# Kernel tuning notes

Measured on AMD Instinct MI355X. Metric: run time of the kernel, lower is better.

## Reference

```python
import jax, jax.numpy as jnp
import numpy as np

KS = 3  # kernel size (mask semantics hardcode 3x3 = 9 taps)


def _xy2d(n, x, y):
    # Hilbert curve: 2D coords -> 1D distance (exact port of HilbertTopology.xy2d)
    d = 0
    s = n // 2
    while s > 0:
        rx = 1 if (x & s) > 0 else 0
        ry = 1 if (y & s) > 0 else 0
        d += s * s * ((3 * rx) ^ ry)
        # rot(s, x, y, rx, ry)
        if ry == 0:
            if rx == 1:
                x = s - 1 - x
                y = s - 1 - y
            x, y = y, x
        s //= 2
    return d


def _build_causal_mask(height, width):
    n = 1
    while n < max(width, height):
        n *= 2
    hgrid = np.empty((height, width), dtype=np.int64)
    for y in range(height):
        for x in range(width):
            hgrid[y, x] = _xy2d(n, x, y)
    # pad with -1 so out-of-bounds neighbors never mask (mask stays 1.0, matching torch code)
    hp = np.pad(hgrid, 1, constant_values=-1)
    mask = np.ones((KS * KS, height, width), dtype=np.float32)
    k = 0
    for dy in range(KS):
        for dx in range(KS):
            nh = hp[dy:dy + height, dx:dx + width]
            mask[k] = np.where(nh > hgrid, 0.0, 1.0)
            k += 1
    return mask[None, None]  # [1, 1, 9, H, W]


def setup_inputs() -> dict:
    key = jax.random.key(0)
    k1, k2 = jax.random.split(key)
    B, C, H, W = 4, 256, 128, 128
    retina = jax.random.normal(k1, (B, C, H, W), dtype=jnp.float32)
    evolve_weight = jax.random.normal(k2, (C, C, KS, KS), dtype=jnp.float32) * 0.05
    causal_mask = jnp.asarray(_build_causal_mask(H, W))
    return {"retina": retina, "evolve_weight": evolve_weight,
            "causal_mask": causal_mask, "steps": 5}


def _spatial_causal_conv(x, evolve_weight, causal_mask):
    B, C, H, W = x.shape
    xp = jnp.pad(x, ((0, 0), (0, 0), (1, 1), (1, 1)))
    # im2col in F.unfold's (dy, dx) tap order -> [B, C, 9, H, W]
    patches = jnp.stack([xp[:, :, dy:dy + H, dx:dx + W]
                         for dy in range(KS) for dx in range(KS)], axis=2)
    masked = patches * causal_mask  # position-dependent causal mask
    w = evolve_weight.reshape(C, C * KS * KS)
    out = jnp.einsum('oj,bjhw->bohw', w, masked.reshape(B, C * KS * KS, H, W))
    return out


def reference(retina, evolve_weight, causal_mask, steps):
    x = retina
    for _ in range(steps):
        delta = _spatial_causal_conv(x, evolve_weight, causal_mask)
        x = x + delta / (1.0 + jnp.abs(delta))  # exact_activation
    return x
```

## Files before the change

kernel.cpp:

```cpp
#include <hip/hip_runtime.h>
#include <math.h>
#include <stdint.h>

#define B_ 4
#define C_ 256
#define H_ 128
#define W_ 128
#define NPIX (H_*W_)

typedef short bf16x8 __attribute__((ext_vector_type(8)));
typedef int   i32x4  __attribute__((ext_vector_type(4)));
typedef float f32x4  __attribute__((ext_vector_type(4)));
typedef float f32x16 __attribute__((ext_vector_type(16)));
typedef unsigned short u16x4 __attribute__((ext_vector_type(4)));

#define XSZ   45056
#define WOFF  XSZ
#define WSL   16384
#define LDS_TOTAL (WOFF + 2*WSL)

__device__ __forceinline__ unsigned short f2bf_rne(float v) {
    uint32_t b = __float_as_uint(v);
    return (unsigned short)((b + 0x7fff + ((b >> 16) & 1)) >> 16);
}
__device__ __forceinline__ float bf2f(unsigned short h) {
    return __uint_as_float(((uint32_t)h) << 16);
}

__global__ __launch_bounds__(256)
void prep_w4(const float* __restrict__ wg, unsigned short* __restrict__ wb4,
             unsigned short* __restrict__ zb) {
    if (blockIdx.x == 2304) { if (threadIdx.x < 128) zb[threadIdx.x] = 0; return; }
    int f = blockIdx.x * 256 + threadIdx.x;
    int s2 = f >> 13;
    int r = f & 8191;
    int o_loc = r >> 6;
    int t = r & 63;
    int up = t >> 3, e = t & 7;
    int oh = s2 / 36, sl = s2 - oh * 36;
    int qt = sl / 9, k = sl - qt * 9;
    int u = up ^ (o_loc & 7);
    int c = qt * 64 + u * 8 + e;
    int o = oh * 128 + o_loc;
    wb4[f] = f2bf_rne(wg[(o * C_ + c) * 9 + k]);
}

__global__ __launch_bounds__(256)
void prep_split(const float* __restrict__ retina, unsigned short* __restrict__ hi,
                unsigned short* __restrict__ lo) {
    __shared__ unsigned int t[64][65];
    int bid = blockIdx.x;
    const int wt = bid & 1;        bid >>= 1;
    const int h  = bid & 127;      bid >>= 7;
    const int ct = bid & 3;        const int b = bid >> 2;
    const int tid = threadIdx.x;
    const int ci4 = tid >> 6, wi = tid & 63;
    #pragma unroll
    for (int cc = 0; cc < 16; ++cc) {
        int c_loc = cc * 4 + ci4;
        float v = retina[((size_t)(b * C_ + ct * 64 + c_loc) * H_ + h) * W_ + wt * 64 + wi];
        unsigned short hv = f2bf_rne(v);
        unsigned short lv = f2bf_rne(v - bf2f(hv));
        t[c_loc][wi] = (unsigned)hv | ((unsigned)lv << 16);
    }
    __syncthreads();
    const int p = tid >> 2, j = tid & 3;
    size_t base = (((size_t)(b * H_ + h) * W_ + wt * 64 + p) << 8) + ct * 64 + j * 16;
    u16x4 hv4[4], lv4[4];
    #pragma unroll
    for (int e = 0; e < 16; ++e) {
        unsigned u = t[j * 16 + e][p];
        hv4[e >> 2][e & 3] = (unsigned short)(u & 0xffffu);
        lv4[e >> 2][e & 3] = (unsigned short)(u >> 16);
    }
    #pragma unroll
    for (int q2 = 0; q2 < 4; ++q2) {
        *(u16x4*)(hi + base + q2 * 4) = hv4[q2];
        *(u16x4*)(lo + base + q2 * 4) = lv4[q2];
    }
}

__device__ __forceinline__ void stage_w(const unsigned short* __restrict__ wb4,
                                        char* smem, int woff, int oh, int sl,
                                        int wid, int l) {
    const char* src = (const char*)wb4 + ((size_t)(oh * 36 + sl) << 14);
    #pragma unroll
    for (int j = 0; j < 4; ++j) {
        const int seg = ((j << 2) + wid) << 10;
        __builtin_amdgcn_global_load_lds(
            (const __attribute__((address_space(1))) uint32_t*)(src + seg + l * 16),
            (__attribute__((address_space(3))) uint32_t*)(smem + woff + seg), 16, 0, 0);
    }
    __builtin_amdgcn_sched_barrier(0);
}

__device__ __forceinline__ void stage_x(const unsigned short* __restrict__ hi_in,
                                        const unsigned short* __restrict__ zb,
                                        char* smem, int b, int tr, int tc,
                                        int qt, int wid, int l) {
    const int slot_r = l >> 3, sub = l & 7;
    #pragma unroll
    for (int op = 0; op < 11; ++op) {
        const int sbase = (op << 5) + (wid << 3);
        const int s = sbase + slot_r;
        const int rr = (s * 3641) >> 16;
        const int hc = s - rr * 18;
        const int h = tr * 16 + rr - 1;
        const int w = tc * 16 + hc - 1;
        const unsigned short* src;
        if (s < 324 && (unsigned)h < 128u && (unsigned)w < 128u)
            src = hi_in + (((size_t)((b * 128 + h) * 128 + w)) << 8) + (qt << 6)
                        + ((sub ^ (s & 7)) << 3);
        else
            src = zb + (sub << 3);
        __builtin_amdgcn_global_load_lds(
            (const __attribute__((address_space(1))) uint32_t*)src,
            (__attribute__((address_space(3))) uint32_t*)(smem + (sbase << 7)),
            16, 0, 0);
    }
    __builtin_amdgcn_sched_barrier(0);
}

__global__ __launch_bounds__(256, 2)
void nca_v10(const unsigned short* __restrict__ hi_in,
             const unsigned short* __restrict__ lo_in,
             const unsigned short* __restrict__ wb4,
             const unsigned short* __restrict__ zb,
             const float* __restrict__ mask,
             unsigned short* __restrict__ hi_out,
             unsigned short* __restrict__ lo_out)
{
    extern __shared__ char smem[];
    const int tid = threadIdx.x;
    const int l = tid & 63, wid = tid >> 6;
    const int wave_o = wid & 1, wp = wid >> 1;
    const int lane31 = l & 31, khalf = l >> 5;
    const int col = l & 15, rowin = (l >> 4) & 1;

    int bid = blockIdx.x;
    const int oh = bid & 1; bid >>= 1;
    const int tc = bid & 7; bid >>= 3;
    const int tr = bid & 7; const int b = bid >> 3;

    unsigned long long mbits = 0ull;
    #pragma unroll
    for (int k = 0; k < 9; ++k) {
        #pragma unroll
        for (int n = 0; n < 4; ++n) {
            const int h = tr * 16 + wp * 8 + n * 2 + rowin;
            const int w = tc * 16 + col;
            unsigned long long bit = (mask[k * NPIX + h * W_ + w] != 0.f) ? 1ull : 0ull;
            mbits |= bit << (k * 4 + n);
        }
    }
    __builtin_amdgcn_sched_barrier(0);

    stage_x(hi_in, zb, smem, b, tr, tc, 0, wid, l);
    stage_w(wb4, smem, WOFF,       oh, 0, wid, l);
    stage_w(wb4, smem, WOFF + WSL, oh, 1, wid, l);

    int sB[4];
    #pragma unroll
    for (int n = 0; n < 4; ++n) sB[n] = (wp * 8 + n * 2 + rowin) * 18 + col;
    int abase[2], aswz[2];
    #pragma unroll
    for (int mo = 0; mo < 2; ++mo) {
        int o_l = wave_o * 64 + mo * 32 + lane31;
        abase[mo] = o_l << 7;
        aswz[mo] = o_l & 7;
    }

    f32x16 zv;
    #pragma unroll
    for (int r = 0; r < 16; ++r) zv[r] = 0.f;
    f32x16 acc[2][4];
    #pragma unroll
    for (int mo = 0; mo < 2; ++mo)
        #pragma unroll
        for (int n = 0; n < 4; ++n) acc[mo][n] = zv;

    #pragma unroll 1
    for (int qt = 0; qt < 4; ++qt) {
        #pragma unroll 1
        for (int k = 0; k < 9; ++k) {
            const int sl = qt * 9 + k;
            if (sl == 35) asm volatile("s_waitcnt vmcnt(0)" ::: "memory");
            else          asm volatile("s_waitcnt vmcnt(4)" ::: "memory");
            __builtin_amdgcn_sched_barrier(0);
            __builtin_amdgcn_s_barrier();

            const int dy = (k * 11) >> 5;
            const int dx = k - dy * 3;
            const int doff = dy * 18 + dx;
            const char* wbuf = smem + WOFF + ((sl & 1) ? WSL : 0);
            const unsigned mk = (unsigned)(mbits >> (k * 4));

            int sx[4];
            #pragma unroll
            for (int n = 0; n < 4; ++n) sx[n] = sB[n] + doff;

            __builtin_amdgcn_s_setprio(1);
            #pragma unroll
            for (int ks = 0; ks < 4; ++ks) {
                const int u = ks * 2 + khalf;
                bf16x8 av[2];
                #pragma unroll
                for (int mo = 0; mo < 2; ++mo)
                    av[mo] = *(const bf16x8*)(wbuf + abase[mo] + ((u ^ aswz[mo]) << 4));
                bf16x8 bv[4];
                #pragma unroll
                for (int n = 0; n < 4; ++n) {
                    i32x4 braw = *(const i32x4*)(smem + (sx[n] << 7) + ((u ^ (sx[n] & 7)) << 4));
                    const int mm = -(int)((mk >> n) & 1u);
                    #pragma unroll
                    for (int w4 = 0; w4 < 4; ++w4) braw[w4] &= mm;
                    bv[n] = __builtin_bit_cast(bf16x8, braw);
                }
                #pragma unroll
                for (int mo = 0; mo < 2; ++mo)
                    #pragma unroll
                    for (int n = 0; n < 4; ++n)
                        acc[mo][n] = __builtin_amdgcn_mfma_f32_32x32x16_bf16(av[mo], bv[n], acc[mo][n], 0, 0, 0);
            }
            __builtin_amdgcn_s_setprio(0);

            asm volatile("" ::: "memory");
            __builtin_amdgcn_s_barrier();
            if (k == 8 && qt < 3)
                stage_x(hi_in, zb, smem, b, tr, tc, qt + 1, wid, l);
            if (sl + 2 < 36)
                stage_w(wb4, smem, WOFF + ((sl & 1) ? WSL : 0), oh, sl + 2, wid, l);
        }
    }

    __syncthreads();
    #pragma unroll 1
    for (int ph = 0; ph < 2; ++ph) {
        #pragma unroll
        for (int n1 = 0; n1 < 2; ++n1) {
            const int n = ph * 2 + n1;
            const int pxp = (wp * 4 + n1 * 2 + ((l & 31) >> 4)) * 16 + col;
            #pragma unroll
            for (int mo = 0; mo < 2; ++mo)
                #pragma unroll
                for (int rq = 0; rq < 4; ++rq) {
                    const int u = wave_o * 16 + mo * 8 + rq * 2 + khalf;
                    f32x4 v;
                    v[0] = acc[mo][n][rq * 4 + 0];
                    v[1] = acc[mo][n][rq * 4 + 1];
                    v[2] = acc[mo][n][rq * 4 + 2];
                    v[3] = acc[mo][n][rq * 4 + 3];
                    *(f32x4*)(smem + pxp * 512 + ((u >> 3) << 7)
                              + ((((u & 7) ^ (u >> 3) ^ (pxp & 7))) << 4)) = v;
                }
        }
        __syncthreads();
        #pragma unroll 2
        for (int it = 0; it < 16; ++it) {
            const int pxp = it * 8 + wid * 2 + (l >> 5);
            const int u = l & 31;
            const f32x4 d4 = *(const f32x4*)(smem + pxp * 512 + ((u >> 3) << 7)
                                             + ((((u & 7) ^ (u >> 3) ^ (pxp & 7))) << 4));
            const int rp = pxp >> 4;
            const int h = tr * 16 + (rp >> 2) * 8 + ph * 4 + (rp & 3);
            const int w = tc * 16 + (pxp & 15);
            const size_t a2 = (((size_t)((b * 128 + h) * 128 + w)) << 8)
                              + (oh << 7) + (size_t)u * 4;
            const u16x4 h4 = *(const u16x4*)(hi_in + a2);
            const u16x4 l4 = *(const u16x4*)(lo_in + a2);
            u16x4 ho, lo2;
            #pragma unroll
            for (int r = 0; r < 4; ++r) {
                const float xv = bf2f(h4[r]) + bf2f(l4[r]);
                const float d = d4[r];
                const float xn = xv + d / (1.f + fabsf(d));
                ho[r] = f2bf_rne(xn);
                lo2[r] = f2bf_rne(xn - bf2f(ho[r]));
            }
            *(u16x4*)(hi_out + a2) = ho;
            *(u16x4*)(lo_out + a2) = lo2;
        }
        if (ph == 0) __syncthreads();
    }
}

__global__ __launch_bounds__(256)
void shadows_to_f32(const unsigned short* __restrict__ hi,
                    const unsigned short* __restrict__ lo,
                    float* __restrict__ out)
{
    __shared__ float t[64][132];
    int bid = blockIdx.x;
    const int ct = bid & 3;  bid >>= 2;
    const int h  = bid & 127; const int b = bid >> 7;
    const int tid = threadIdx.x;
    #pragma unroll
    for (int pass = 0; pass < 8; ++pass) {
        const int w = pass * 16 + (tid >> 4);
        const int c0 = (tid & 15) * 4;
        const size_t base = (((size_t)((b * 128 + h) * 128 + w)) << 8) + ct * 64 + c0;
        const u16x4 hv = *(const u16x4*)(hi + base);
        const u16x4 lv = *(const u16x4*)(lo + base);
        #pragma unroll
        for (int e = 0; e < 4; ++e) t[c0 + e][w] = bf2f(hv[e]) + bf2f(lv[e]);
    }
    __syncthreads();
    #pragma unroll
    for (int pass = 0; pass < 8; ++pass) {
        const int c = pass * 8 + (tid >> 5);
        const int w = (tid & 31) * 4;
        float4 v = make_float4(t[c][w], t[c][w + 1], t[c][w + 2], t[c][w + 3]);
        *(float4*)(out + ((size_t)(b * C_ + ct * 64 + c) * H_ + h) * W_ + w) = v;
    }
}

#define OT 64
#define TR 4
#define TC 16
#define CKC 16
__global__ __launch_bounds__(256)
void nca_step_f32(const float* __restrict__ xin, const float* __restrict__ wg,
                  const float* __restrict__ mask, float* __restrict__ xout)
{
    __shared__ __align__(16) float w_s[CKC][9][OT];
    __shared__ __align__(16) float x_s[CKC][TR + 2][20];
    const int tid = threadIdx.x;
    int bt = blockIdx.x;
    const int col_tile = bt & 7;  bt >>= 3;
    const int row_tile = bt & 31; bt >>= 5;
    const int ot = bt & 3;        const int b = bt >> 2;
    const int gr0 = row_tile * TR, gc0 = col_tile * TC, o_base = ot * OT;
    const int og = tid >> 4, pg = tid & 15;
    const int prow = pg >> 2, pcol4 = (pg & 3) * 4;
    const int orow = gr0 + prow, ocol0 = gc0 + pcol4;
    float mask_r[9][4];
#pragma unroll
    for (int k = 0; k < 9; ++k)
#pragma unroll
        for (int j = 0; j < 4; ++j)
            mask_r[k][j] = mask[k * NPIX + orow * W_ + (ocol0 + j)];
    float acc[4][4];
#pragma unroll
    for (int a = 0; a < 4; ++a)
#pragma unroll
        for (int j = 0; j < 4; ++j) acc[a][j] = 0.f;
    for (int chunk = 0; chunk < C_ / CKC; ++chunk) {
        const int c0 = chunk * CKC;
#pragma unroll
        for (int i = 0; i < 36; ++i) {
            const int flat = i * 256 + tid;
            const int o_l = flat / 144;
            const int r = flat - o_l * 144;
            const int c_l = r / 9;
            const int kk = r - c_l * 9;
            w_s[c_l][kk][o_l] = wg[(o_base + o_l) * (C_ * 9) + (c0 + c_l) * 9 + kk];
        }
#pragma unroll
        for (int i = 0; i < 7; ++i) {
            const int flat = i * 256 + tid;
            if (flat < CKC * 108) {
                const int c_l = flat / 108;
                const int r = flat - c_l * 108;
                const int row = r / 18, colx = r - row * 18;
                const int grow = gr0 - 1 + row, gcol = gc0 - 1 + colx;
                float v = 0.f;
                if ((unsigned)grow < (unsigned)H_ && (unsigned)gcol < (unsigned)W_)
                    v = xin[((b * C_ + c0 + c_l) * H_ + grow) * W_ + gcol];
                x_s[c_l][row][colx] = v;
            }
        }
        __syncthreads();
#pragma unroll
        for (int dyy = 0; dyy < 3; ++dyy) {
            float acck[3][4][4];
#pragma unroll
            for (int dxx = 0; dxx < 3; ++dxx)
#pragma unroll
                for (int a = 0; a < 4; ++a)
#pragma unroll
                    for (int j = 0; j < 4; ++j) acck[dxx][a][j] = 0.f;
#pragma unroll 4
            for (int c = 0; c < CKC; ++c) {
                const float4 xv4 = *(const float4*)&x_s[c][prow + dyy][pcol4];
                const float2 xv2 = *(const float2*)&x_s[c][prow + dyy][pcol4 + 4];
                const float xv[6] = {xv4.x, xv4.y, xv4.z, xv4.w, xv2.x, xv2.y};
#pragma unroll
                for (int dxx = 0; dxx < 3; ++dxx) {
                    const float4 wv = *(const float4*)&w_s[c][dyy * 3 + dxx][og * 4];
                    const float wa[4] = {wv.x, wv.y, wv.z, wv.w};
#pragma unroll
                    for (int a = 0; a < 4; ++a)
#pragma unroll
                        for (int j = 0; j < 4; ++j)
                            acck[dxx][a][j] = fmaf(wa[a], xv[j + dxx], acck[dxx][a][j]);
                }
            }
#pragma unroll
            for (int dxx = 0; dxx < 3; ++dxx) {
                const int k = dyy * 3 + dxx;
#pragma unroll
                for (int a = 0; a < 4; ++a)
#pragma unroll
                    for (int j = 0; j < 4; ++j)
                        acc[a][j] = fmaf(mask_r[k][j], acck[dxx][a][j], acc[a][j]);
            }
        }
        __syncthreads();
    }
#pragma unroll
    for (int a = 0; a < 4; ++a) {
        const int o = o_base + og * 4 + a;
#pragma unroll
        for (int j = 0; j < 4; ++j) {
            const int idx = ((b * C_ + o) * H_ + orow) * W_ + (ocol0 + j);
            const float d = acc[a][j];
            xout[idx] = xin[idx] + d / (1.0f + fabsf(d));
        }
    }
}

extern "C" void kernel_launch(void* const* d_in, const int* in_sizes, int n_in,
                              void* d_out, int out_size, void* d_ws, size_t ws_size,
                              hipStream_t stream) {
    const float* retina = (const float*)d_in[0];
    const float* wg     = (const float*)d_in[1];
    const float* mask   = (const float*)d_in[2];
    float* out = (float*)d_out;

    const size_t need = 0x4200000;

    if (ws_size >= need) {
        unsigned short* wb4 = (unsigned short*)d_ws;
        unsigned short* zb  = (unsigned short*)((char*)d_ws + 0x120000);
        unsigned short* hiA = (unsigned short*)((char*)d_ws + 0x200000);
        unsigned short* loA = (unsigned short*)((char*)d_ws + 0x2200000);
        unsigned short* hiB = (unsigned short*)d_out;
        unsigned short* loB = hiB + (size_t)B_ * NPIX * C_;

        hipFuncSetAttribute((const void*)nca_v10,
                            hipFuncAttributeMaxDynamicSharedMemorySize, LDS_TOTAL);

        prep_w4<<<2305, 256, 0, stream>>>(wg, wb4, zb);
        prep_split<<<4096, 256, 0, stream>>>(retina, hiB, loB);

        nca_v10<<<512, 256, LDS_TOTAL, stream>>>(hiB, loB, wb4, zb, mask, hiA, loA);
        nca_v10<<<512, 256, LDS_TOTAL, stream>>>(hiA, loA, wb4, zb, mask, hiB, loB);
        nca_v10<<<512, 256, LDS_TOTAL, stream>>>(hiB, loB, wb4, zb, mask, hiA, loA);
        nca_v10<<<512, 256, LDS_TOTAL, stream>>>(hiA, loA, wb4, zb, mask, hiB, loB);
        nca_v10<<<512, 256, LDS_TOTAL, stream>>>(hiB, loB, wb4, zb, mask, hiA, loA);
        shadows_to_f32<<<2048, 256, 0, stream>>>(hiA, loA, out);
    } else {
        float* ws = (float*)d_ws;
        const int nblocks = B_ * (C_ / OT) * (H_ / TR) * (W_ / TC);
        const float* src = retina;
        float* dsts[5] = {out, ws, out, ws, out};
        for (int s = 0; s < 5; ++s) {
            nca_step_f32<<<dim3(nblocks), dim3(256), 0, stream>>>(src, wg, mask, dsts[s]);
            src = dsts[s];
        }
    }
}
```

Baseline: 585.2 us.

## Merge output-channel halves into one 512-thread block with per-wave weight buffers

Result: faster. 510.4 us (-12.8%).

```diff
diff --git a/kernel.cpp b/kernel.cpp
--- a/kernel.cpp
+++ b/kernel.cpp
@@ -14,10 +14,10 @@
 typedef float f32x16 __attribute__((ext_vector_type(16)));
 typedef unsigned short u16x4 __attribute__((ext_vector_type(4)));
 
-#define XSZ   45056
-#define WOFF  XSZ
-#define WSL   16384
-#define LDS_TOTAL (WOFF + 2*WSL)
+#define XSZ   41984
+#define WREG  (2*XSZ)
+#define SCR   (WREG + 8*8192)
+#define LDS_TOTAL (SCR + 1024)
 
 __device__ __forceinline__ unsigned short f2bf_rne(float v) {
     uint32_t b = __float_as_uint(v);
@@ -28,21 +28,24 @@
 }
 
 __global__ __launch_bounds__(256)
-void prep_w4(const float* __restrict__ wg, unsigned short* __restrict__ wb4,
+void prep_w5(const float* __restrict__ wg, unsigned short* __restrict__ wb5,
              unsigned short* __restrict__ zb) {
     if (blockIdx.x == 2304) { if (threadIdx.x < 128) zb[threadIdx.x] = 0; return; }
     int f = blockIdx.x * 256 + threadIdx.x;
-    int s2 = f >> 13;
-    int r = f & 8191;
-    int o_loc = r >> 6;
-    int t = r & 63;
-    int up = t >> 3, e = t & 7;
-    int oh = s2 / 36, sl = s2 - oh * 36;
-    int qt = sl / 9, k = sl - qt * 9;
-    int u = up ^ (o_loc & 7);
-    int c = qt * 64 + u * 8 + e;
-    int o = oh * 128 + o_loc;
-    wb4[f] = f2bf_rne(wg[(o * C_ + c) * 9 + k]);
+    int g = f >> 11;
+    int within = f & 2047;
+    int row = within >> 6;
+    int t = within & 63;
+    int vp = t >> 3, e = t & 7;
+    int v = vp ^ (row & 7);
+    int o_loc = row * 2 + (v >> 2);
+    int ua = v & 3;
+    int sl = g >> 2, og = g & 3;
+    int qt = sl / 18, j = sl - qt * 18;
+    int k = j >> 1, chalf = j & 1;
+    int c = qt * 64 + chalf * 32 + ua * 8 + e;
+    int o = og * 64 + o_loc;
+    wb5[f] = f2bf_rne(wg[(o * C_ + c) * 9 + k]);
 }
 
 __global__ __launch_bounds__(256)
@@ -80,16 +83,15 @@
     }
 }
 
-__device__ __forceinline__ void stage_w(const unsigned short* __restrict__ wb4,
-                                        char* smem, int woff, int oh, int sl,
-                                        int wid, int l) {
-    const char* src = (const char*)wb4 + ((size_t)(oh * 36 + sl) << 14);
-    #pragma unroll
-    for (int j = 0; j < 4; ++j) {
-        const int seg = ((j << 2) + wid) << 10;
+__device__ __forceinline__ void stage_wv(const unsigned short* __restrict__ wb5,
+                                         char* smem, int og, int wid, int sl, int l) {
+    const char* src = (const char*)wb5 + ((size_t)(sl * 4 + og) << 12);
+    char* dst = smem + WREG + (wid << 13) + ((sl & 1) << 12);
+    #pragma unroll
+    for (int op = 0; op < 4; ++op) {
         __builtin_amdgcn_global_load_lds(
-            (const __attribute__((address_space(1))) uint32_t*)(src + seg + l * 16),
-            (__attribute__((address_space(3))) uint32_t*)(smem + woff + seg), 16, 0, 0);
+            (const __attribute__((address_space(1))) uint32_t*)(src + (op << 10) + l * 16),
+            (__attribute__((address_space(3))) uint32_t*)(dst + (op << 10)), 16, 0, 0);
     }
     __builtin_amdgcn_sched_barrier(0);
 }
@@ -99,32 +101,39 @@
                                         char* smem, int b, int tr, int tc,
                                         int qt, int wid, int l) {
     const int slot_r = l >> 3, sub = l & 7;
-    #pragma unroll
-    for (int op = 0; op < 11; ++op) {
-        const int sbase = (op << 5) + (wid << 3);
+    const int xoff = (qt & 1) ? XSZ : 0;
+    #pragma unroll
+    for (int op = 0; op < 6; ++op) {
+        const int sbase = ((op << 3) + wid) << 3;
         const int s = sbase + slot_r;
         const int rr = (s * 3641) >> 16;
         const int hc = s - rr * 18;
         const int h = tr * 16 + rr - 1;
         const int w = tc * 16 + hc - 1;
         const unsigned short* src;
-        if (s < 324 && (unsigned)h < 128u && (unsigned)w < 128u)
-            src = hi_in + (((size_t)((b * 128 + h) * 128 + w)) << 8) + (qt << 6)
-                        + ((sub ^ (s & 7)) << 3);
-        else
+        int dst;
+        if (sbase < 328) {
+            dst = xoff + (sbase << 7);
+            if (s < 324 && (unsigned)h < 128u && (unsigned)w < 128u)
+                src = hi_in + (((size_t)((b * 128 + h) * 128 + w)) << 8) + (qt << 6)
+                            + ((sub ^ (s & 7)) << 3);
+            else
+                src = zb + (sub << 3);
+        } else {
+            dst = SCR;
             src = zb + (sub << 3);
+        }
         __builtin_amdgcn_global_load_lds(
             (const __attribute__((address_space(1))) uint32_t*)src,
-            (__attribute__((address_space(3))) uint32_t*)(smem + (sbase << 7)),
-            16, 0, 0);
+            (__attribute__((address_space(3))) uint32_t*)(smem + dst), 16, 0, 0);
     }
     __builtin_amdgcn_sched_barrier(0);
 }
 
-__global__ __launch_bounds__(256, 2)
-void nca_v10(const unsigned short* __restrict__ hi_in,
+__global__ __launch_bounds__(512, 1)
+void nca_v11(const unsigned short* __restrict__ hi_in,
              const unsigned short* __restrict__ lo_in,
-             const unsigned short* __restrict__ wb4,
+             const unsigned short* __restrict__ wb5,
              const unsigned short* __restrict__ zb,
              const float* __restrict__ mask,
              unsigned short* __restrict__ hi_out,
@@ -133,12 +142,11 @@
     extern __shared__ char smem[];
     const int tid = threadIdx.x;
     const int l = tid & 63, wid = tid >> 6;
-    const int wave_o = wid & 1, wp = wid >> 1;
+    const int og = wid & 3, ph = wid >> 2;
     const int lane31 = l & 31, khalf = l >> 5;
     const int col = l & 15, rowin = (l >> 4) & 1;
 
     int bid = blockIdx.x;
-    const int oh = bid & 1; bid >>= 1;
     const int tc = bid & 7; bid >>= 3;
     const int tr = bid & 7; const int b = bid >> 3;
 
@@ -147,7 +155,7 @@
     for (int k = 0; k < 9; ++k) {
         #pragma unroll
         for (int n = 0; n < 4; ++n) {
-            const int h = tr * 16 + wp * 8 + n * 2 + rowin;
+            const int h = tr * 16 + ph * 8 + n * 2 + rowin;
             const int w = tc * 16 + col;
             unsigned long long bit = (mask[k * NPIX + h * W_ + w] != 0.f) ? 1ull : 0ull;
             mbits |= bit << (k * 4 + n);
@@ -156,18 +164,19 @@
     __builtin_amdgcn_sched_barrier(0);
 
     stage_x(hi_in, zb, smem, b, tr, tc, 0, wid, l);
-    stage_w(wb4, smem, WOFF,       oh, 0, wid, l);
-    stage_w(wb4, smem, WOFF + WSL, oh, 1, wid, l);
+    stage_wv(wb5, smem, og, wid, 0, l);
+    stage_wv(wb5, smem, og, wid, 1, l);
 
     int sB[4];
     #pragma unroll
-    for (int n = 0; n < 4; ++n) sB[n] = (wp * 8 + n * 2 + rowin) * 18 + col;
-    int abase[2], aswz[2];
+    for (int n = 0; n < 4; ++n) sB[n] = (ph * 8 + n * 2 + rowin) * 18 + col;
+    int arow[2], asel[2], aswz[2];
     #pragma unroll
     for (int mo = 0; mo < 2; ++mo) {
-        int o_l = wave_o * 64 + mo * 32 + lane31;
-        abase[mo] = o_l << 7;
-        aswz[mo] = o_l & 7;
+        int o_loc = mo * 32 + lane31;
+        arow[mo] = (o_loc >> 1) << 7;
+        asel[mo] = (o_loc & 1) << 2;
+        aswz[mo] = (o_loc >> 1) & 7;
     }
 
     f32x16 zv;
@@ -180,94 +189,96 @@
         for (int n = 0; n < 4; ++n) acc[mo][n] = zv;
 
     #pragma unroll 1
-    for (int qt = 0; qt < 4; ++qt) {
-        #pragma unroll 1
-        for (int k = 0; k < 9; ++k) {
-            const int sl = qt * 9 + k;
-            if (sl == 35) asm volatile("s_waitcnt vmcnt(0)" ::: "memory");
-            else          asm volatile("s_waitcnt vmcnt(4)" ::: "memory");
+    for (int sl = 0; sl < 72; ++sl) {
+        const int qt = sl / 18;
+        const int j = sl - qt * 18;
+        const int k = j >> 1, chalf = j & 1;
+
+        if (j == 0 && qt > 0) {
+            asm volatile("s_waitcnt vmcnt(8)" ::: "memory");
             __builtin_amdgcn_sched_barrier(0);
             __builtin_amdgcn_s_barrier();
-
-            const int dy = (k * 11) >> 5;
-            const int dx = k - dy * 3;
-            const int doff = dy * 18 + dx;
-            const char* wbuf = smem + WOFF + ((sl & 1) ? WSL : 0);
-            const unsigned mk = (unsigned)(mbits >> (k * 4));
-
-            int sx[4];
+        }
+        if (sl == 71)             asm volatile("s_waitcnt vmcnt(0)"  ::: "memory");
+        else if (j == 1 && qt < 3) asm volatile("s_waitcnt vmcnt(10)" ::: "memory");
+        else                      asm volatile("s_waitcnt vmcnt(4)"  ::: "memory");
+        __builtin_amdgcn_sched_barrier(0);
+
+        const int dy = (k * 11) >> 5;
+        const int dx = k - dy * 3;
+        const int doff = dy * 18 + dx;
+        const char* xbuf = smem + ((qt & 1) ? XSZ : 0);
+        const char* wbuf = smem + WREG + (wid << 13) + ((sl & 1) << 12);
+        const unsigned mk = (unsigned)(mbits >> (k * 4));
+
+        int sx[4];
+        #pragma unroll
+        for (int n = 0; n < 4; ++n) sx[n] = sB[n] + doff;
+
+        __builtin_amdgcn_s_setprio(1);
+        #pragma unroll
+        for (int k2 = 0; k2 < 2; ++k2) {
+            const int ua = k2 * 2 + khalf;
+            const int ub = chalf * 4 + ua;
+            bf16x8 av[2];
             #pragma unroll
-            for (int n = 0; n < 4; ++n) sx[n] = sB[n] + doff;
-
-            __builtin_amdgcn_s_setprio(1);
+            for (int mo = 0; mo < 2; ++mo)
+                av[mo] = *(const bf16x8*)(wbuf + arow[mo] + (((asel[mo] + ua) ^ aswz[mo]) << 4));
+            bf16x8 bv[4];
             #pragma unroll
-            for (int ks = 0; ks < 4; ++ks) {
-                const int u = ks * 2 + khalf;
-                bf16x8 av[2];
+            for (int n = 0; n < 4; ++n) {
+                i32x4 braw = *(const i32x4*)(xbuf + (sx[n] << 7) + ((ub ^ (sx[n] & 7)) << 4));
+                const int mm = -(int)((mk >> n) & 1u);
                 #pragma unroll
-                for (int mo = 0; mo < 2; ++mo)
-                    av[mo] = *(const bf16x8*)(wbuf + abase[mo] + ((u ^ aswz[mo]) << 4));
-                bf16x8 bv[4];
+                for (int w4 = 0; w4 < 4; ++w4) braw[w4] &= mm;
+                bv[n] = __builtin_bit_cast(bf16x8, braw);
+            }
+            #pragma unroll
+            for (int mo = 0; mo < 2; ++mo)
                 #pragma unroll
-                for (int n = 0; n < 4; ++n) {
-                    i32x4 braw = *(const i32x4*)(smem + (sx[n] << 7) + ((u ^ (sx[n] & 7)) << 4));
-                    const int mm = -(int)((mk >> n) & 1u);
-                    #pragma unroll
-                    for (int w4 = 0; w4 < 4; ++w4) braw[w4] &= mm;
-                    bv[n] = __builtin_bit_cast(bf16x8, braw);
-                }
+                for (int n = 0; n < 4; ++n)
+                    acc[mo][n] = __builtin_amdgcn_mfma_f32_32x32x16_bf16(av[mo], bv[n], acc[mo][n], 0, 0, 0);
+        }
+        __builtin_amdgcn_s_setprio(0);
+
+        __builtin_amdgcn_sched_barrier(0);
+        if (j == 0 && qt < 3)
+            stage_x(hi_in, zb, smem, b, tr, tc, qt + 1, wid, l);
+        if (sl + 2 < 72)
+            stage_wv(wb5, smem, og, wid, sl + 2, l);
+    }
+
+    __syncthreads();
+    #pragma unroll 1
+    for (int f = 0; f < 2; ++f) {
+        if (ph == f) {
+            #pragma unroll
+            for (int n = 0; n < 4; ++n) {
+                const int pl = (n * 2 + rowin) * 16 + col;
                 #pragma unroll
                 for (int mo = 0; mo < 2; ++mo)
                     #pragma unroll
-                    for (int n = 0; n < 4; ++n)
-                        acc[mo][n] = __builtin_amdgcn_mfma_f32_32x32x16_bf16(av[mo], bv[n], acc[mo][n], 0, 0, 0);
-            }
-            __builtin_amdgcn_s_setprio(0);
-
-            asm volatile("" ::: "memory");
-            __builtin_amdgcn_s_barrier();
-            if (k == 8 && qt < 3)
-                stage_x(hi_in, zb, smem, b, tr, tc, qt + 1, wid, l);
-            if (sl + 2 < 36)
-                stage_w(wb4, smem, WOFF + ((sl & 1) ? WSL : 0), oh, sl + 2, wid, l);
-        }
-    }
-
-    __syncthreads();
-    #pragma unroll 1
-    for (int ph = 0; ph < 2; ++ph) {
-        #pragma unroll
-        for (int n1 = 0; n1 < 2; ++n1) {
-            const int n = ph * 2 + n1;
-            const int pxp = (wp * 4 + n1 * 2 + ((l & 31) >> 4)) * 16 + col;
-            #pragma unroll
-            for (int mo = 0; mo < 2; ++mo)
-                #pragma unroll
-                for (int rq = 0; rq < 4; ++rq) {
-                    const int u = wave_o * 16 + mo * 8 + rq * 2 + khalf;
-                    f32x4 v;
-                    v[0] = acc[mo][n][rq * 4 + 0];
-                    v[1] = acc[mo][n][rq * 4 + 1];
-                    v[2] = acc[mo][n][rq * 4 + 2];
-                    v[3] = acc[mo][n][rq * 4 + 3];
-                    *(f32x4*)(smem + pxp * 512 + ((u >> 3) << 7)
-                              + ((((u & 7) ^ (u >> 3) ^ (pxp & 7))) << 4)) = v;
-                }
+                    for (int rq = 0; rq < 4; ++rq) {
+                        const int u = og * 16 + mo * 8 + rq * 2 + khalf;
+                        f32x4 v;
+                        v[0] = acc[mo][n][rq * 4 + 0];
+                        v[1] = acc[mo][n][rq * 4 + 1];
+                        v[2] = acc[mo][n][rq * 4 + 2];
+                        v[3] = acc[mo][n][rq * 4 + 3];
+                        *(f32x4*)(smem + pl * 1024 + ((u ^ (pl & 7)) << 4)) = v;
+                    }
+            }
         }
         __syncthreads();
         #pragma unroll 2
         for (int it = 0; it < 16; ++it) {
-            const int pxp = it * 8 + wid * 2 + (l >> 5);
-            const int u = l & 31;
-            const f32x4 d4 = *(const f32x4*)(smem + pxp * 512 + ((u >> 3) << 7)
-                                             + ((((u & 7) ^ (u >> 3) ^ (pxp & 7))) << 4));
-            const int rp = pxp >> 4;
-            const int h = tr * 16 + (rp >> 2) * 8 + ph * 4 + (rp & 3);
-            const int w = tc * 16 + (pxp & 15);
-            const size_t a2 = (((size_t)((b * 128 + h) * 128 + w)) << 8)
-                              + (oh << 7) + (size_t)u * 4;
-            const u16x4 h4 = *(const u16x4*)(hi_in + a2);
-            const u16x4 l4 = *(const u16x4*)(lo_in + a2);
+            const int pl = it * 8 + wid;
+            const int h = tr * 16 + f * 8 + (pl >> 4);
+            const int w = tc * 16 + (pl & 15);
+            const f32x4 d4 = *(const f32x4*)(smem + pl * 1024 + ((l ^ wid) << 4));
+            const size_t base = (((size_t)((b * 128 + h) * 128 + w)) << 8) + l * 4;
+            const u16x4 h4 = *(const u16x4*)(hi_in + base);
+            const u16x4 l4 = *(const u16x4*)(lo_in + base);
             u16x4 ho, lo2;
             #pragma unroll
             for (int r = 0; r < 4; ++r) {
@@ -277,10 +288,10 @@
                 ho[r] = f2bf_rne(xn);
                 lo2[r] = f2bf_rne(xn - bf2f(ho[r]));
             }
-            *(u16x4*)(hi_out + a2) = ho;
-            *(u16x4*)(lo_out + a2) = lo2;
-        }
-        if (ph == 0) __syncthreads();
+            *(u16x4*)(hi_out + base) = ho;
+            *(u16x4*)(lo_out + base) = lo2;
+        }
+        if (f == 0) __syncthreads();
     }
 }
 
@@ -430,24 +441,24 @@
     const size_t need = 0x4200000;
 
     if (ws_size >= need) {
-        unsigned short* wb4 = (unsigned short*)d_ws;
+        unsigned short* wb5 = (unsigned short*)d_ws;
         unsigned short* zb  = (unsigned short*)((char*)d_ws + 0x120000);
         unsigned short* hiA = (unsigned short*)((char*)d_ws + 0x200000);
         unsigned short* loA = (unsigned short*)((char*)d_ws + 0x2200000);
         unsigned short* hiB = (unsigned short*)d_out;
         unsigned short* loB = hiB + (size_t)B_ * NPIX * C_;
 
-        hipFuncSetAttribute((const void*)nca_v10,
+        hipFuncSetAttribute((const void*)nca_v11,
                             hipFuncAttributeMaxDynamicSharedMemorySize, LDS_TOTAL);
 
-        prep_w4<<<2305, 256, 0, stream>>>(wg, wb4, zb);
+        prep_w5<<<2305, 256, 0, stream>>>(wg, wb5, zb);
         prep_split<<<4096, 256, 0, stream>>>(retina, hiB, loB);
 
-        nca_v10<<<512, 256, LDS_TOTAL, stream>>>(hiB, loB, wb4, zb, mask, hiA, loA);
-        nca_v10<<<512, 256, LDS_TOTAL, stream>>>(hiA, loA, wb4, zb, mask, hiB, loB);
-        nca_v10<<<512, 256, LDS_TOTAL, stream>>>(hiB, loB, wb4, zb, mask, hiA, loA);
-        nca_v10<<<512, 256, LDS_TOTAL, stream>>>(hiA, loA, wb4, zb, mask, hiB, loB);
-        nca_v10<<<512, 256, LDS_TOTAL, stream>>>(hiB, loB, wb4, zb, mask, hiA, loA);
+        nca_v11<<<256, 512, LDS_TOTAL, stream>>>(hiB, loB, wb5, zb, mask, hiA, loA);
+        nca_v11<<<256, 512, LDS_TOTAL, stream>>>(hiA, loA, wb5, zb, mask, hiB, loB);
+        nca_v11<<<256, 512, LDS_TOTAL, stream>>>(hiB, loB, wb5, zb, mask, hiA, loA);
+        nca_v11<<<256, 512, LDS_TOTAL, stream>>>(hiA, loA, wb5, zb, mask, hiB, loB);
+        nca_v11<<<256, 512, LDS_TOTAL, stream>>>(hiB, loB, wb5, zb, mask, hiA, loA);
         shadows_to_f32<<<2048, 256, 0, stream>>>(hiA, loA, out);
     } else {
         float* ws = (float*)d_ws;
```
